# Performance work log

Hardware: AMD Instinct MI355X
Metric: run time of the kernel (lower is better)

## Reference

```python
import jax, jax.numpy as jnp
import numpy as np

B, N, H = 2, 2048, 256
NUM_HEADS = 8
HEAD_DIM = H // NUM_HEADS
E = 65536
NEG = -1e30
LN_EPS = 1e-5


def setup_inputs() -> dict:
    key = jax.random.key(0)
    ks = jax.random.split(key, 8)
    x = jax.random.normal(ks[0], (B, N, H), dtype=jnp.float32)
    edge_index = jax.random.randint(ks[1], (2, E), 0, N, dtype=jnp.int32)
    edge_weights = jax.random.uniform(ks[2], (E,), dtype=jnp.float32)
    s = 1.0 / np.sqrt(H)
    Wq = jax.random.normal(ks[3], (H, H), dtype=jnp.float32) * s
    Wk = jax.random.normal(ks[4], (H, H), dtype=jnp.float32) * s
    Wv = jax.random.normal(ks[5], (H, H), dtype=jnp.float32) * s
    Wo = jax.random.normal(ks[6], (H, H), dtype=jnp.float32) * s
    ln_gamma = jnp.ones((H,), dtype=jnp.float32)
    ln_beta = jnp.zeros((H,), dtype=jnp.float32)
    return {"node_embeddings": x, "edge_index": edge_index, "edge_weights": edge_weights,
            "Wq": Wq, "Wk": Wk, "Wv": Wv, "Wo": Wo, "ln_gamma": ln_gamma, "ln_beta": ln_beta}


def reference(node_embeddings, edge_index, edge_weights, Wq, Wk, Wv, Wo, ln_gamma, ln_beta):
    x = node_embeddings
    residual = x
    # torch Linear: y = x @ W.T
    def proj(W):
        y = jnp.einsum('bnd,ed->bne', x, W)
        return y.reshape(B, N, NUM_HEADS, HEAD_DIM).transpose(0, 2, 1, 3)  # [B,h,N,hd]
    Q, K, V = proj(Wq), proj(Wk), proj(Wv)
    scale = 1.0 / jnp.sqrt(jnp.float32(HEAD_DIM))
    scores = jnp.einsum('bhnd,bhmd->bhnm', Q, K) * scale  # [B,h,N,N]
    # adjacency mask from edge list
    mask = jnp.zeros((N, N), dtype=bool).at[edge_index[0], edge_index[1]].set(True)
    scores = jnp.where(mask[None, None], scores, NEG)
    w = jax.nn.softmax(scores, axis=-1)
    # rows with no edges: softmax over uniform NEG -> uniform; multiply by mask zeroes them
    # (equivalent to torch's -inf softmax + nan->0, but grad-safe)
    w = w * mask[None, None].astype(w.dtype)
    attn = jnp.einsum('bhnm,bhmd->bhnd', w, V)
    attn = attn.transpose(0, 2, 1, 3).reshape(B, N, H)
    out = jnp.einsum('bnd,ed->bne', attn, Wo)
    y = out + residual
    mu = jnp.mean(y, axis=-1, keepdims=True)
    var = jnp.mean(jnp.square(y - mu), axis=-1, keepdims=True)
    y = (y - mu) / jnp.sqrt(var + LN_EPS) * ln_gamma + ln_beta
    return y
```

## Files before the change

kernel.cpp:

```cpp
#include <hip/hip_runtime.h>
#include <math.h>

#define Bb 2
#define Nn 2048
#define Hh 256
#define NH 8
#define HD 32
#define NEDGE 65536
#define LN_EPS 1e-5f
#define MW 64

typedef __bf16 bf16_t;
typedef bf16_t bf16x8 __attribute__((ext_vector_type(8)));
typedef bf16_t bf16x4 __attribute__((ext_vector_type(4)));
typedef float f32x4 __attribute__((ext_vector_type(4)));

__global__ void build_mask_kernel(const int* __restrict__ ei, unsigned int* __restrict__ mask) {
    int e = blockIdx.x * blockDim.x + threadIdx.x;
    if (e >= NEDGE) return;
    int src = ei[e];
    int dst = ei[NEDGE + e];
    atomicOr(&mask[src * MW + (dst >> 5)], 1u << (dst & 31));
}

__global__ __launch_bounds__(256) void cvt_zero_kernel(
    const float* __restrict__ s0, const float* __restrict__ s1, const float* __restrict__ s2,
    const float* __restrict__ s3, const float* __restrict__ s4,
    bf16_t* __restrict__ d0, bf16_t* __restrict__ d1, bf16_t* __restrict__ d2,
    bf16_t* __restrict__ d3, bf16_t* __restrict__ d4,
    uint4* __restrict__ mask4)
{
    int which = blockIdx.y;
    int i = blockIdx.x * blockDim.x + threadIdx.x;
    if (which == 5) {
        if (i < Nn * MW / 4) mask4[i] = make_uint4(0, 0, 0, 0);
        return;
    }
    const float* s = (which == 0) ? s0 : (which == 1) ? s1 : (which == 2) ? s2 : (which == 3) ? s3 : s4;
    bf16_t* d = (which == 0) ? d0 : (which == 1) ? d1 : (which == 2) ? d2 : (which == 3) ? d3 : d4;
    int n4 = (which == 0) ? (Bb * Nn * Hh / 4) : (Hh * Hh / 4);
    if (i >= n4) return;
    float4 v = ((const float4*)s)[i];
    bf16x4 o = {(bf16_t)v.x, (bf16_t)v.y, (bf16_t)v.z, (bf16_t)v.w};
    ((bf16x4*)d)[i] = o;
}

#define LDA2 72

__global__ __launch_bounds__(256) void qkv_gemm3_kernel(
    const bf16_t* __restrict__ xb,
    const bf16_t* __restrict__ Wqb, const bf16_t* __restrict__ Wkb, const bf16_t* __restrict__ Wvb,
    float* __restrict__ Qb, bf16_t* __restrict__ Kb16, bf16_t* __restrict__ Vb16)
{
    __shared__ bf16_t As[64 * LDA2];
    __shared__ bf16_t Ws[64 * LDA2];
    int t = threadIdx.x;
    int lane = t & 63, w = t >> 6;
    int wm = w & 1, wn = w >> 1;
    int ml = lane & 15, quad = lane >> 4;
    int m0 = blockIdx.x * 64;
    int wsel = blockIdx.y >> 2;
    const bf16_t* W = (wsel == 0) ? Wqb : ((wsel == 1) ? Wkb : Wvb);
    int n0 = (blockIdx.y & 3) * 64;
    int srow = t >> 3;
    int scol = (t & 7) * 8;
    f32x4 acc[2][2];
    f32x4 zero = {0.f, 0.f, 0.f, 0.f};
    acc[0][0] = zero; acc[0][1] = zero; acc[1][0] = zero; acc[1][1] = zero;

    for (int k0 = 0; k0 < Hh; k0 += 64) {
        bf16x8 a[2], b[2];
        #pragma unroll
        for (int s = 0; s < 2; ++s) {
            a[s] = *(const bf16x8*)(xb + (size_t)(m0 + srow + s * 32) * Hh + k0 + scol);
            b[s] = *(const bf16x8*)(W  + (size_t)(n0 + srow + s * 32) * Hh + k0 + scol);
        }
        __syncthreads();
        #pragma unroll
        for (int s = 0; s < 2; ++s) {
            *(bf16x8*)&As[(srow + s * 32) * LDA2 + scol] = a[s];
            *(bf16x8*)&Ws[(srow + s * 32) * LDA2 + scol] = b[s];
        }
        __syncthreads();
        #pragma unroll
        for (int kk = 0; kk < 64; kk += 32) {
            bf16x8 af[2], bfr[2];
            #pragma unroll
            for (int i = 0; i < 2; ++i) {
                af[i]  = *(const bf16x8*)&As[(wm * 32 + i * 16 + ml) * LDA2 + kk + quad * 8];
                bfr[i] = *(const bf16x8*)&Ws[(wn * 32 + i * 16 + ml) * LDA2 + kk + quad * 8];
            }
            #pragma unroll
            for (int i = 0; i < 2; ++i)
                #pragma unroll
                for (int j = 0; j < 2; ++j)
                    acc[i][j] = __builtin_amdgcn_mfma_f32_16x16x32_bf16(af[i], bfr[j], acc[i][j], 0, 0, 0);
        }
    }
    bf16_t* Ob16 = (wsel == 1) ? Kb16 : Vb16;
    #pragma unroll
    for (int i = 0; i < 2; ++i)
        #pragma unroll
        for (int j = 0; j < 2; ++j)
            #pragma unroll
            for (int r = 0; r < 4; ++r) {
                int mg = m0 + wm * 32 + i * 16 + quad * 4 + r;
                int ng = n0 + wn * 32 + j * 16 + ml;
                float v = acc[i][j][r];
                if (wsel == 0) Qb[(size_t)mg * Hh + ng] = v;
                else           Ob16[(size_t)mg * Hh + ng] = (bf16_t)v;
            }
}

__global__ __launch_bounds__(256) void attn5_kernel(
    const float* __restrict__ Qb, const bf16_t* __restrict__ Kb16, const bf16_t* __restrict__ Vb16,
    const unsigned int* __restrict__ mask, float* __restrict__ attnb)
{
    __shared__ unsigned short nbr[Nn];
    __shared__ float qs[Hh];
    __shared__ float sraw[32 * 9];
    __shared__ float scw[Hh];
    __shared__ float alpha_l[NH];
    __shared__ float linv_l[NH];
    __shared__ float obuf[4][Hh];
    __shared__ int nn_sh;
    int gid = blockIdx.x;
    int i = gid & (Nn - 1);
    int b = gid >> 11;
    int t = threadIdx.x;
    int h = t >> 5, dl = t & 31;
    int w = t >> 6, lane = t & 63;
    int hw = lane >> 3;

    if (t < 64) {
        unsigned int bits = mask[i * MW + t];
        int cnt = __popc(bits);
        int incl = cnt;
        #pragma unroll
        for (int off = 1; off < 64; off <<= 1) {
            int v = __shfl_up(incl, off, 64);
            if (t >= off) incl += v;
        }
        int idx = incl - cnt;
        unsigned int bb = bits;
        while (bb) {
            int bit = __ffs(bb) - 1;
            nbr[idx++] = (unsigned short)(t * 32 + bit);
            bb &= bb - 1;
        }
        if (t == 63) nn_sh = incl;
    }
    qs[t] = Qb[((size_t)((b << 11) + i)) * Hh + t];
    __syncthreads();
    int nn = nn_sh;

    float m_run = -1e30f, l_run = 0.f;
    float o0 = 0.f, o1 = 0.f, o2 = 0.f, o3 = 0.f;
    const float scale = 0.17677669529663687f;
    int nch = (nn + 31) >> 5;
    for (int c = 0; c < nch; ++c) {
        int base = c << 5;
        int lim = min(32, nn - base);
        float4 qv = *(const float4*)&qs[lane << 2];
        #pragma unroll
        for (int s = 0; s < 8; ++s) {
            int r = (s << 2) + w;
            if (r < lim) {
                int j = nbr[base + r];
                bf16x4 kv = *(const bf16x4*)(Kb16 + (((size_t)((b << 11) + j)) << 8) + (lane << 2));
                float p = fmaf((float)kv.x, qv.x, fmaf((float)kv.y, qv.y,
                          fmaf((float)kv.z, qv.z, (float)kv.w * qv.w)));
                p += __shfl_xor(p, 1, 64);
                p += __shfl_xor(p, 2, 64);
                p += __shfl_xor(p, 4, 64);
                if ((lane & 7) == 0) sraw[r * 9 + (lane >> 3)] = p * scale;
            }
        }
        __syncthreads();
        float s_val = (dl < lim) ? sraw[dl * 9 + h] : -1e30f;
        float mc = s_val;
        #pragma unroll
        for (int m = 1; m < 32; m <<= 1) mc = fmaxf(mc, __shfl_xor(mc, m, 64));
        float m_new = fmaxf(m_run, mc);
        float wgt = __expf(s_val - m_new);
        float sum = wgt;
        #pragma unroll
        for (int m = 1; m < 32; m <<= 1) sum += __shfl_xor(sum, m, 64);
        float alpha = __expf(m_run - m_new);
        l_run = l_run * alpha + sum;
        m_run = m_new;
        scw[t] = wgt;
        if (dl == 0) alpha_l[h] = alpha;
        __syncthreads();
        float av = alpha_l[hw];
        o0 *= av; o1 *= av; o2 *= av; o3 *= av;
        #pragma unroll
        for (int s = 0; s < 8; ++s) {
            int r = (s << 2) + w;
            if (r < lim) {
                int j = nbr[base + r];
                float wg = scw[(hw << 5) + r];
                bf16x4 vv = *(const bf16x4*)(Vb16 + (((size_t)((b << 11) + j)) << 8) + (lane << 2));
                o0 = fmaf(wg, (float)vv.x, o0);
                o1 = fmaf(wg, (float)vv.y, o1);
                o2 = fmaf(wg, (float)vv.z, o2);
                o3 = fmaf(wg, (float)vv.w, o3);
            }
        }
    }
    if (dl == 0) linv_l[h] = (l_run > 0.f) ? 1.f / l_run : 0.f;
    obuf[w][(lane << 2) + 0] = o0;
    obuf[w][(lane << 2) + 1] = o1;
    obuf[w][(lane << 2) + 2] = o2;
    obuf[w][(lane << 2) + 3] = o3;
    __syncthreads();
    float val = obuf[0][t] + obuf[1][t] + obuf[2][t] + obuf[3][t];
    attnb[(((size_t)((b << 11) + i)) << 8) + t] = val * linv_l[t >> 5];
}

__global__ __launch_bounds__(256) void out_ln_kernel(
    const float* __restrict__ attnb, const bf16_t* __restrict__ Wob,
    const float* __restrict__ x, const float* __restrict__ gamma,
    const float* __restrict__ beta, float* __restrict__ out)
{
    __shared__ bf16_t As[16 * LDA2];
    __shared__ __align__(16) char wbuf[256 * LDA2 * sizeof(bf16_t)];
    bf16_t* Ws = (bf16_t*)wbuf;
    float* yb = (float*)wbuf;
    int t = threadIdx.x;
    int lane = t & 63, w = t >> 6;
    int ml = lane & 15, quad = lane >> 4;
    int m0 = blockIdx.x * 16;
    f32x4 acc[4];
    f32x4 zero = {0.f, 0.f, 0.f, 0.f};
    acc[0] = zero; acc[1] = zero; acc[2] = zero; acc[3] = zero;
    int arow = t >> 4, acol = (t & 15) * 4;
    int wrow = t >> 3, wcol = (t & 7) * 8;

    for (int k0 = 0; k0 < Hh; k0 += 64) {
        float4 av = *(const float4*)(attnb + (size_t)(m0 + arow) * Hh + k0 + acol);
        bf16x8 wv[8];
        #pragma unroll
        for (int s = 0; s < 8; ++s)
            wv[s] = *(const bf16x8*)(Wob + (size_t)(wrow + s * 32) * Hh + k0 + wcol);
        __syncthreads();
        bf16x4 ac = {(bf16_t)av.x, (bf16_t)av.y, (bf16_t)av.z, (bf16_t)av.w};
        *(bf16x4*)&As[arow * LDA2 + acol] = ac;
        #pragma unroll
        for (int s = 0; s < 8; ++s)
            *(bf16x8*)&Ws[(wrow + s * 32) * LDA2 + wcol] = wv[s];
        __syncthreads();
        #pragma unroll
        for (int kk = 0; kk < 64; kk += 32) {
            bf16x8 af = *(const bf16x8*)&As[ml * LDA2 + kk + quad * 8];
            #pragma unroll
            for (int ct = 0; ct < 4; ++ct) {
                bf16x8 bfr = *(const bf16x8*)&Ws[(w * 64 + ct * 16 + ml) * LDA2 + kk + quad * 8];
                acc[ct] = __builtin_amdgcn_mfma_f32_16x16x32_bf16(af, bfr, acc[ct], 0, 0, 0);
            }
        }
    }
    __syncthreads();
    #pragma unroll
    for (int ct = 0; ct < 4; ++ct)
        #pragma unroll
        for (int r = 0; r < 4; ++r) {
            int row = quad * 4 + r;
            int col = w * 64 + ct * 16 + ml;
            yb[row * 260 + col] = acc[ct][r] + x[(size_t)(m0 + row) * Hh + col];
        }
    __syncthreads();
    for (int rr = 0; rr < 4; ++rr) {
        int row = w * 4 + rr;
        float4 v = *(const float4*)&yb[row * 260 + lane * 4];
        float sum = v.x + v.y + v.z + v.w;
        #pragma unroll
        for (int m = 1; m < 64; m <<= 1) sum += __shfl_xor(sum, m, 64);
        float mu = sum * (1.f / Hh);
        float4 d = {v.x - mu, v.y - mu, v.z - mu, v.w - mu};
        float ss = d.x * d.x + d.y * d.y + d.z * d.z + d.w * d.w;
        #pragma unroll
        for (int m = 1; m < 64; m <<= 1) ss += __shfl_xor(ss, m, 64);
        float r = rsqrtf(ss * (1.f / Hh) + LN_EPS);
        float4 g  = *(const float4*)(gamma + lane * 4);
        float4 bt = *(const float4*)(beta + lane * 4);
        float4 ov = {d.x * r * g.x + bt.x, d.y * r * g.y + bt.y,
                     d.z * r * g.z + bt.z, d.w * r * g.w + bt.w};
        *(float4*)(out + (size_t)(m0 + row) * Hh + lane * 4) = ov;
    }
}

extern "C" void kernel_launch(void* const* d_in, const int* in_sizes, int n_in,
                              void* d_out, int out_size, void* d_ws, size_t ws_size,
                              hipStream_t stream) {
    const float* x     = (const float*)d_in[0];
    const int*   ei    = (const int*)d_in[1];
    const float* Wq    = (const float*)d_in[3];
    const float* Wk    = (const float*)d_in[4];
    const float* Wv    = (const float*)d_in[5];
    const float* Wo    = (const float*)d_in[6];
    const float* gamma = (const float*)d_in[7];
    const float* beta  = (const float*)d_in[8];
    float* out = (float*)d_out;

    const int NTOK = Bb * Nn * Hh;
    float*  Qb    = (float*)d_ws;
    bf16_t* Kb16  = (bf16_t*)(Qb + NTOK);
    bf16_t* Vb16  = Kb16 + NTOK;
    float*  attnb = (float*)(Vb16 + NTOK);
    unsigned int* mask = (unsigned int*)(attnb + NTOK);
    bf16_t* xb  = (bf16_t*)(mask + Nn * MW);
    bf16_t* Wqb = xb + NTOK;
    bf16_t* Wkb = Wqb + Hh * Hh;
    bf16_t* Wvb = Wkb + Hh * Hh;
    bf16_t* Wob = Wvb + Hh * Hh;

    hipLaunchKernelGGL(cvt_zero_kernel, dim3(NTOK / 4 / 256, 6), dim3(256), 0, stream,
                       x, Wq, Wk, Wv, Wo, xb, Wqb, Wkb, Wvb, Wob, (uint4*)mask);
    hipLaunchKernelGGL(build_mask_kernel, dim3(NEDGE / 256), dim3(256), 0, stream, ei, mask);
    hipLaunchKernelGGL(qkv_gemm3_kernel, dim3((Bb * Nn) / 64, 12), dim3(256), 0, stream,
                       xb, Wqb, Wkb, Wvb, Qb, Kb16, Vb16);
    hipLaunchKernelGGL(attn5_kernel, dim3(Bb * Nn), dim3(256), 0, stream,
                       Qb, Kb16, Vb16, mask, attnb);
    hipLaunchKernelGGL(out_ln_kernel, dim3((Bb * Nn) / 16), dim3(256), 0, stream,
                       attnb, Wob, x, gamma, beta, out);
}
```

Measured before the change: 116.5 us.

## Fuse mask build into QKV GEMM and attention with output projection and LayerNorm

The separate mask-building kernel is folded into the QKV GEMM, with each thread doing one edge atomicOr before its GEMM work. The attention kernel now handles 4 query rows per block, keeps the attention outputs in LDS, and then runs the Wo projection plus residual and LayerNorm in the same block. This removes the attnb global round trip and two launches. Attention chunks grow from 32 to 64 neighbours. In exchange there are only 1024 attention blocks instead of 4096, rows are processed serially inside a block, and Wo is reloaded per block for an M=4 MFMA tile that wastes 3/4 of each 16-row tile.

```diff
diff --git a/kernel.cpp b/kernel.cpp
--- a/kernel.cpp
+++ b/kernel.cpp
@@ -5,23 +5,15 @@
 #define Nn 2048
 #define Hh 256
 #define NH 8
-#define HD 32
 #define NEDGE 65536
 #define LN_EPS 1e-5f
 #define MW 64
+#define LDA2 72
 
 typedef __bf16 bf16_t;
 typedef bf16_t bf16x8 __attribute__((ext_vector_type(8)));
 typedef bf16_t bf16x4 __attribute__((ext_vector_type(4)));
 typedef float f32x4 __attribute__((ext_vector_type(4)));
-
-__global__ void build_mask_kernel(const int* __restrict__ ei, unsigned int* __restrict__ mask) {
-    int e = blockIdx.x * blockDim.x + threadIdx.x;
-    if (e >= NEDGE) return;
-    int src = ei[e];
-    int dst = ei[NEDGE + e];
-    atomicOr(&mask[src * MW + (dst >> 5)], 1u << (dst & 31));
-}
 
 __global__ __launch_bounds__(256) void cvt_zero_kernel(
     const float* __restrict__ s0, const float* __restrict__ s1, const float* __restrict__ s2,
@@ -45,16 +37,21 @@
     ((bf16x4*)d)[i] = o;
 }
 
-#define LDA2 72
-
-__global__ __launch_bounds__(256) void qkv_gemm3_kernel(
+__global__ __launch_bounds__(256) void qkv_gemm_mask_kernel(
     const bf16_t* __restrict__ xb,
     const bf16_t* __restrict__ Wqb, const bf16_t* __restrict__ Wkb, const bf16_t* __restrict__ Wvb,
-    float* __restrict__ Qb, bf16_t* __restrict__ Kb16, bf16_t* __restrict__ Vb16)
+    float* __restrict__ Qb, bf16_t* __restrict__ Kb16, bf16_t* __restrict__ Vb16,
+    const int* __restrict__ ei, unsigned int* __restrict__ mask)
 {
     __shared__ bf16_t As[64 * LDA2];
     __shared__ bf16_t Ws[64 * LDA2];
     int t = threadIdx.x;
+    int linb = blockIdx.y * 64 + blockIdx.x;
+    int gtid = linb * 256 + t;
+    if (gtid < NEDGE) {
+        int src = ei[gtid], dst = ei[NEDGE + gtid];
+        atomicOr(&mask[src * MW + (dst >> 5)], 1u << (dst & 31));
+    }
     int lane = t & 63, w = t >> 6;
     int wm = w & 1, wn = w >> 1;
     int ml = lane & 15, quad = lane >> 4;
@@ -65,214 +62,222 @@
     int srow = t >> 3;
     int scol = (t & 7) * 8;
     f32x4 acc[2][2];
-    f32x4 zero = {0.f, 0.f, 0.f, 0.f};
-    acc[0][0] = zero; acc[0][1] = zero; acc[1][0] = zero; acc[1][1] = zero;
+    f32x4 zf = {0.f, 0.f, 0.f, 0.f};
+    acc[0][0] = zf; acc[0][1] = zf; acc[1][0] = zf; acc[1][1] = zf;
 
     for (int k0 = 0; k0 < Hh; k0 += 64) {
-        bf16x8 a[2], b[2];
-        #pragma unroll
-        for (int s = 0; s < 2; ++s) {
-            a[s] = *(const bf16x8*)(xb + (size_t)(m0 + srow + s * 32) * Hh + k0 + scol);
-            b[s] = *(const bf16x8*)(W  + (size_t)(n0 + srow + s * 32) * Hh + k0 + scol);
-        }
-        __syncthreads();
-        #pragma unroll
-        for (int s = 0; s < 2; ++s) {
-            *(bf16x8*)&As[(srow + s * 32) * LDA2 + scol] = a[s];
-            *(bf16x8*)&Ws[(srow + s * 32) * LDA2 + scol] = b[s];
-        }
+        bf16x8 a0 = *(const bf16x8*)(xb + (size_t)(m0 + srow) * Hh + k0 + scol);
+        bf16x8 a1 = *(const bf16x8*)(xb + (size_t)(m0 + srow + 32) * Hh + k0 + scol);
+        bf16x8 b0 = *(const bf16x8*)(W + (size_t)(n0 + srow) * Hh + k0 + scol);
+        bf16x8 b1 = *(const bf16x8*)(W + (size_t)(n0 + srow + 32) * Hh + k0 + scol);
+        __syncthreads();
+        *(bf16x8*)&As[srow * LDA2 + scol] = a0;
+        *(bf16x8*)&As[(srow + 32) * LDA2 + scol] = a1;
+        *(bf16x8*)&Ws[srow * LDA2 + scol] = b0;
+        *(bf16x8*)&Ws[(srow + 32) * LDA2 + scol] = b1;
         __syncthreads();
         #pragma unroll
         for (int kk = 0; kk < 64; kk += 32) {
             bf16x8 af[2], bfr[2];
             #pragma unroll
-            for (int i = 0; i < 2; ++i) {
-                af[i]  = *(const bf16x8*)&As[(wm * 32 + i * 16 + ml) * LDA2 + kk + quad * 8];
-                bfr[i] = *(const bf16x8*)&Ws[(wn * 32 + i * 16 + ml) * LDA2 + kk + quad * 8];
-            }
-            #pragma unroll
-            for (int i = 0; i < 2; ++i)
+            for (int i2 = 0; i2 < 2; ++i2) {
+                af[i2]  = *(const bf16x8*)&As[(wm * 32 + i2 * 16 + ml) * LDA2 + kk + quad * 8];
+                bfr[i2] = *(const bf16x8*)&Ws[(wn * 32 + i2 * 16 + ml) * LDA2 + kk + quad * 8];
+            }
+            #pragma unroll
+            for (int i2 = 0; i2 < 2; ++i2)
                 #pragma unroll
-                for (int j = 0; j < 2; ++j)
-                    acc[i][j] = __builtin_amdgcn_mfma_f32_16x16x32_bf16(af[i], bfr[j], acc[i][j], 0, 0, 0);
-        }
-    }
-    bf16_t* Ob16 = (wsel == 1) ? Kb16 : Vb16;
+                for (int j2 = 0; j2 < 2; ++j2)
+                    acc[i2][j2] = __builtin_amdgcn_mfma_f32_16x16x32_bf16(af[i2], bfr[j2], acc[i2][j2], 0, 0, 0);
+        }
+    }
     #pragma unroll
-    for (int i = 0; i < 2; ++i)
-        #pragma unroll
-        for (int j = 0; j < 2; ++j)
+    for (int i2 = 0; i2 < 2; ++i2)
+        #pragma unroll
+        for (int j2 = 0; j2 < 2; ++j2)
             #pragma unroll
             for (int r = 0; r < 4; ++r) {
-                int mg = m0 + wm * 32 + i * 16 + quad * 4 + r;
-                int ng = n0 + wn * 32 + j * 16 + ml;
-                float v = acc[i][j][r];
-                if (wsel == 0) Qb[(size_t)mg * Hh + ng] = v;
-                else           Ob16[(size_t)mg * Hh + ng] = (bf16_t)v;
+                int mg = m0 + wm * 32 + i2 * 16 + quad * 4 + r;
+                int ng = n0 + wn * 32 + j2 * 16 + ml;
+                float v = acc[i2][j2][r];
+                if (wsel == 0)      Qb[(size_t)mg * Hh + ng] = v;
+                else if (wsel == 1) Kb16[(size_t)mg * Hh + ng] = (bf16_t)v;
+                else                Vb16[(size_t)mg * Hh + ng] = (bf16_t)v;
             }
 }
 
-__global__ __launch_bounds__(256) void attn5_kernel(
+struct AttnLds {
+    float aout[4][Hh];
+    unsigned short nbr[Nn];
+    float qs[Hh];
+    float sraw[64 * 9];
+    float scw2[NH * 64];
+    float alpha_l[NH];
+    float linv_l[NH];
+    float obuf[4][Hh];
+    int nn_sh;
+};
+struct OlnLds {
+    float aout[4][Hh];
+    union { bf16_t Ws[64 * 136]; float yb[4][260]; } u2;
+};
+union FusedLds { AttnLds a; OlnLds o; };
+
+__global__ __launch_bounds__(256) void attn_out_ln_kernel(
     const float* __restrict__ Qb, const bf16_t* __restrict__ Kb16, const bf16_t* __restrict__ Vb16,
-    const unsigned int* __restrict__ mask, float* __restrict__ attnb)
-{
-    __shared__ unsigned short nbr[Nn];
-    __shared__ float qs[Hh];
-    __shared__ float sraw[32 * 9];
-    __shared__ float scw[Hh];
-    __shared__ float alpha_l[NH];
-    __shared__ float linv_l[NH];
-    __shared__ float obuf[4][Hh];
-    __shared__ int nn_sh;
-    int gid = blockIdx.x;
-    int i = gid & (Nn - 1);
-    int b = gid >> 11;
-    int t = threadIdx.x;
-    int h = t >> 5, dl = t & 31;
-    int w = t >> 6, lane = t & 63;
-    int hw = lane >> 3;
-
-    if (t < 64) {
-        unsigned int bits = mask[i * MW + t];
-        int cnt = __popc(bits);
-        int incl = cnt;
-        #pragma unroll
-        for (int off = 1; off < 64; off <<= 1) {
-            int v = __shfl_up(incl, off, 64);
-            if (t >= off) incl += v;
-        }
-        int idx = incl - cnt;
-        unsigned int bb = bits;
-        while (bb) {
-            int bit = __ffs(bb) - 1;
-            nbr[idx++] = (unsigned short)(t * 32 + bit);
-            bb &= bb - 1;
-        }
-        if (t == 63) nn_sh = incl;
-    }
-    qs[t] = Qb[((size_t)((b << 11) + i)) * Hh + t];
-    __syncthreads();
-    int nn = nn_sh;
-
-    float m_run = -1e30f, l_run = 0.f;
-    float o0 = 0.f, o1 = 0.f, o2 = 0.f, o3 = 0.f;
-    const float scale = 0.17677669529663687f;
-    int nch = (nn + 31) >> 5;
-    for (int c = 0; c < nch; ++c) {
-        int base = c << 5;
-        int lim = min(32, nn - base);
-        float4 qv = *(const float4*)&qs[lane << 2];
-        #pragma unroll
-        for (int s = 0; s < 8; ++s) {
-            int r = (s << 2) + w;
-            if (r < lim) {
-                int j = nbr[base + r];
-                bf16x4 kv = *(const bf16x4*)(Kb16 + (((size_t)((b << 11) + j)) << 8) + (lane << 2));
-                float p = fmaf((float)kv.x, qv.x, fmaf((float)kv.y, qv.y,
-                          fmaf((float)kv.z, qv.z, (float)kv.w * qv.w)));
-                p += __shfl_xor(p, 1, 64);
-                p += __shfl_xor(p, 2, 64);
-                p += __shfl_xor(p, 4, 64);
-                if ((lane & 7) == 0) sraw[r * 9 + (lane >> 3)] = p * scale;
-            }
-        }
-        __syncthreads();
-        float s_val = (dl < lim) ? sraw[dl * 9 + h] : -1e30f;
-        float mc = s_val;
-        #pragma unroll
-        for (int m = 1; m < 32; m <<= 1) mc = fmaxf(mc, __shfl_xor(mc, m, 64));
-        float m_new = fmaxf(m_run, mc);
-        float wgt = __expf(s_val - m_new);
-        float sum = wgt;
-        #pragma unroll
-        for (int m = 1; m < 32; m <<= 1) sum += __shfl_xor(sum, m, 64);
-        float alpha = __expf(m_run - m_new);
-        l_run = l_run * alpha + sum;
-        m_run = m_new;
-        scw[t] = wgt;
-        if (dl == 0) alpha_l[h] = alpha;
-        __syncthreads();
-        float av = alpha_l[hw];
-        o0 *= av; o1 *= av; o2 *= av; o3 *= av;
-        #pragma unroll
-        for (int s = 0; s < 8; ++s) {
-            int r = (s << 2) + w;
-            if (r < lim) {
-                int j = nbr[base + r];
-                float wg = scw[(hw << 5) + r];
-                bf16x4 vv = *(const bf16x4*)(Vb16 + (((size_t)((b << 11) + j)) << 8) + (lane << 2));
-                o0 = fmaf(wg, (float)vv.x, o0);
-                o1 = fmaf(wg, (float)vv.y, o1);
-                o2 = fmaf(wg, (float)vv.z, o2);
-                o3 = fmaf(wg, (float)vv.w, o3);
-            }
-        }
-    }
-    if (dl == 0) linv_l[h] = (l_run > 0.f) ? 1.f / l_run : 0.f;
-    obuf[w][(lane << 2) + 0] = o0;
-    obuf[w][(lane << 2) + 1] = o1;
-    obuf[w][(lane << 2) + 2] = o2;
-    obuf[w][(lane << 2) + 3] = o3;
-    __syncthreads();
-    float val = obuf[0][t] + obuf[1][t] + obuf[2][t] + obuf[3][t];
-    attnb[(((size_t)((b << 11) + i)) << 8) + t] = val * linv_l[t >> 5];
-}
-
-__global__ __launch_bounds__(256) void out_ln_kernel(
-    const float* __restrict__ attnb, const bf16_t* __restrict__ Wob,
+    const unsigned int* __restrict__ mask, const bf16_t* __restrict__ Wob,
     const float* __restrict__ x, const float* __restrict__ gamma,
     const float* __restrict__ beta, float* __restrict__ out)
 {
-    __shared__ bf16_t As[16 * LDA2];
-    __shared__ __align__(16) char wbuf[256 * LDA2 * sizeof(bf16_t)];
-    bf16_t* Ws = (bf16_t*)wbuf;
-    float* yb = (float*)wbuf;
-    int t = threadIdx.x;
+    __shared__ FusedLds u;
+    int blk = blockIdx.x, t = threadIdx.x;
     int lane = t & 63, w = t >> 6;
     int ml = lane & 15, quad = lane >> 4;
-    int m0 = blockIdx.x * 16;
-    f32x4 acc[4];
-    f32x4 zero = {0.f, 0.f, 0.f, 0.f};
-    acc[0] = zero; acc[1] = zero; acc[2] = zero; acc[3] = zero;
-    int arow = t >> 4, acol = (t & 15) * 4;
-    int wrow = t >> 3, wcol = (t & 7) * 8;
-
-    for (int k0 = 0; k0 < Hh; k0 += 64) {
-        float4 av = *(const float4*)(attnb + (size_t)(m0 + arow) * Hh + k0 + acol);
-        bf16x8 wv[8];
-        #pragma unroll
-        for (int s = 0; s < 8; ++s)
-            wv[s] = *(const bf16x8*)(Wob + (size_t)(wrow + s * 32) * Hh + k0 + wcol);
-        __syncthreads();
-        bf16x4 ac = {(bf16_t)av.x, (bf16_t)av.y, (bf16_t)av.z, (bf16_t)av.w};
-        *(bf16x4*)&As[arow * LDA2 + acol] = ac;
-        #pragma unroll
-        for (int s = 0; s < 8; ++s)
-            *(bf16x8*)&Ws[(wrow + s * 32) * LDA2 + wcol] = wv[s];
-        __syncthreads();
-        #pragma unroll
-        for (int kk = 0; kk < 64; kk += 32) {
-            bf16x8 af = *(const bf16x8*)&As[ml * LDA2 + kk + quad * 8];
-            #pragma unroll
-            for (int ct = 0; ct < 4; ++ct) {
-                bf16x8 bfr = *(const bf16x8*)&Ws[(w * 64 + ct * 16 + ml) * LDA2 + kk + quad * 8];
-                acc[ct] = __builtin_amdgcn_mfma_f32_16x16x32_bf16(af, bfr, acc[ct], 0, 0, 0);
-            }
-        }
+    int h = t >> 5, dl = t & 31;
+    int hw = lane >> 3;
+    const float scale = 0.17677669529663687f;
+
+    for (int rr = 0; rr < 4; ++rr) {
+        int ri = blk * 4 + rr;
+        int b = ri >> 11, i = ri & (Nn - 1);
+        __syncthreads();
+        if (t < 64) {
+            unsigned int bits = mask[i * MW + t];
+            int cnt = __popc(bits);
+            int incl = cnt;
+            #pragma unroll
+            for (int off = 1; off < 64; off <<= 1) {
+                int v = __shfl_up(incl, off, 64);
+                if (t >= off) incl += v;
+            }
+            int idx = incl - cnt;
+            unsigned int bb = bits;
+            while (bb) {
+                int bit = __ffs(bb) - 1;
+                u.a.nbr[idx++] = (unsigned short)(t * 32 + bit);
+                bb &= bb - 1;
+            }
+            if (t == 63) u.a.nn_sh = incl;
+        }
+        u.a.qs[t] = Qb[(size_t)ri * Hh + t];
+        __syncthreads();
+        int nn = u.a.nn_sh;
+
+        float m_run = -1e30f, l_run = 0.f;
+        float o0 = 0.f, o1 = 0.f, o2 = 0.f, o3 = 0.f;
+        int nch = (nn + 63) >> 6;
+        for (int c = 0; c < nch; ++c) {
+            int base = c << 6;
+            int lim = min(64, nn - base);
+            float4 qv = *(const float4*)&u.a.qs[lane << 2];
+            #pragma unroll
+            for (int s = 0; s < 16; ++s) {
+                int r = (s << 2) + w;
+                if (r < lim) {
+                    int j = u.a.nbr[base + r];
+                    bf16x4 kv = *(const bf16x4*)(Kb16 + (((size_t)((b << 11) + j)) << 8) + (lane << 2));
+                    float p = fmaf((float)kv.x, qv.x, fmaf((float)kv.y, qv.y,
+                              fmaf((float)kv.z, qv.z, (float)kv.w * qv.w)));
+                    p += __shfl_xor(p, 1, 64);
+                    p += __shfl_xor(p, 2, 64);
+                    p += __shfl_xor(p, 4, 64);
+                    if ((lane & 7) == 0) u.a.sraw[r * 9 + (lane >> 3)] = p * scale;
+                }
+            }
+            __syncthreads();
+            float s0 = (dl < lim) ? u.a.sraw[dl * 9 + h] : -1e30f;
+            float s1 = (dl + 32 < lim) ? u.a.sraw[(dl + 32) * 9 + h] : -1e30f;
+            float mc = fmaxf(s0, s1);
+            #pragma unroll
+            for (int m = 1; m < 32; m <<= 1) mc = fmaxf(mc, __shfl_xor(mc, m, 64));
+            float m_new = fmaxf(m_run, mc);
+            float w0 = __expf(s0 - m_new), w1 = __expf(s1 - m_new);
+            float sum = w0 + w1;
+            #pragma unroll
+            for (int m = 1; m < 32; m <<= 1) sum += __shfl_xor(sum, m, 64);
+            float alpha = __expf(m_run - m_new);
+            l_run = l_run * alpha + sum;
+            m_run = m_new;
+            u.a.scw2[h * 64 + dl] = w0;
+            u.a.scw2[h * 64 + dl + 32] = w1;
+            if (dl == 0) u.a.alpha_l[h] = alpha;
+            __syncthreads();
+            float av = u.a.alpha_l[hw];
+            o0 *= av; o1 *= av; o2 *= av; o3 *= av;
+            #pragma unroll
+            for (int s = 0; s < 16; ++s) {
+                int r = (s << 2) + w;
+                if (r < lim) {
+                    int j = u.a.nbr[base + r];
+                    float wg = u.a.scw2[hw * 64 + r];
+                    bf16x4 vv = *(const bf16x4*)(Vb16 + (((size_t)((b << 11) + j)) << 8) + (lane << 2));
+                    o0 = fmaf(wg, (float)vv.x, o0);
+                    o1 = fmaf(wg, (float)vv.y, o1);
+                    o2 = fmaf(wg, (float)vv.z, o2);
+                    o3 = fmaf(wg, (float)vv.w, o3);
+                }
+            }
+            __syncthreads();
+        }
+        if (dl == 0) u.a.linv_l[h] = (l_run > 0.f) ? 1.f / l_run : 0.f;
+        u.a.obuf[w][(lane << 2) + 0] = o0;
+        u.a.obuf[w][(lane << 2) + 1] = o1;
+        u.a.obuf[w][(lane << 2) + 2] = o2;
+        u.a.obuf[w][(lane << 2) + 3] = o3;
+        __syncthreads();
+        float val = u.a.obuf[0][t] + u.a.obuf[1][t] + u.a.obuf[2][t] + u.a.obuf[3][t];
+        u.a.aout[rr][t] = val * u.a.linv_l[t >> 5];
     }
     __syncthreads();
-    #pragma unroll
-    for (int ct = 0; ct < 4; ++ct)
-        #pragma unroll
-        for (int r = 0; r < 4; ++r) {
-            int row = quad * 4 + r;
-            int col = w * 64 + ct * 16 + ml;
-            yb[row * 260 + col] = acc[ct][r] + x[(size_t)(m0 + row) * Hh + col];
-        }
-    __syncthreads();
-    for (int rr = 0; rr < 4; ++rr) {
-        int row = w * 4 + rr;
-        float4 v = *(const float4*)&yb[row * 260 + lane * 4];
+
+    {
+        int mlr = ml & 3;
+        bf16x8 af[8];
+        #pragma unroll
+        for (int kc = 0; kc < 8; ++kc) {
+            float4 a0 = *(const float4*)&u.o.aout[mlr][kc * 32 + quad * 8];
+            float4 a1 = *(const float4*)&u.o.aout[mlr][kc * 32 + quad * 8 + 4];
+            bf16x8 f = {(bf16_t)a0.x, (bf16_t)a0.y, (bf16_t)a0.z, (bf16_t)a0.w,
+                        (bf16_t)a1.x, (bf16_t)a1.y, (bf16_t)a1.z, (bf16_t)a1.w};
+            af[kc] = f;
+        }
+        int wr = t >> 2, wc = (t & 3) * 32;
+        f32x4 acc[4];
+        f32x4 zf = {0.f, 0.f, 0.f, 0.f};
+        acc[0] = zf; acc[1] = zf; acc[2] = zf; acc[3] = zf;
+        #pragma unroll
+        for (int nc = 0; nc < 4; ++nc) {
+            #pragma unroll
+            for (int kcp = 0; kcp < 2; ++kcp) {
+                bf16x8 wv0 = *(const bf16x8*)(Wob + (size_t)(nc * 64 + wr) * Hh + kcp * 128 + wc);
+                bf16x8 wv1 = *(const bf16x8*)(Wob + (size_t)(nc * 64 + wr) * Hh + kcp * 128 + wc + 8);
+                bf16x8 wv2 = *(const bf16x8*)(Wob + (size_t)(nc * 64 + wr) * Hh + kcp * 128 + wc + 16);
+                bf16x8 wv3 = *(const bf16x8*)(Wob + (size_t)(nc * 64 + wr) * Hh + kcp * 128 + wc + 24);
+                __syncthreads();
+                *(bf16x8*)&u.o.u2.Ws[wr * 136 + wc +  0] = wv0;
+                *(bf16x8*)&u.o.u2.Ws[wr * 136 + wc +  8] = wv1;
+                *(bf16x8*)&u.o.u2.Ws[wr * 136 + wc + 16] = wv2;
+                *(bf16x8*)&u.o.u2.Ws[wr * 136 + wc + 24] = wv3;
+                __syncthreads();
+                #pragma unroll
+                for (int k2 = 0; k2 < 4; ++k2) {
+                    bf16x8 bfr = *(const bf16x8*)&u.o.u2.Ws[(w * 16 + ml) * 136 + k2 * 32 + quad * 8];
+                    acc[nc] = __builtin_amdgcn_mfma_f32_16x16x32_bf16(af[kcp * 4 + k2], bfr, acc[nc], 0, 0, 0);
+                }
+            }
+        }
+        __syncthreads();
+        if (quad == 0) {
+            #pragma unroll
+            for (int nc = 0; nc < 4; ++nc)
+                #pragma unroll
+                for (int r = 0; r < 4; ++r) {
+                    int col = nc * 64 + w * 16 + ml;
+                    u.o.u2.yb[r][col] = acc[nc][r] + x[(size_t)(blk * 4 + r) * Hh + col];
+                }
+        }
+        __syncthreads();
+        float4 v = *(const float4*)&u.o.u2.yb[w][lane * 4];
         float sum = v.x + v.y + v.z + v.w;
         #pragma unroll
         for (int m = 1; m < 64; m <<= 1) sum += __shfl_xor(sum, m, 64);
@@ -286,7 +291,7 @@
         float4 bt = *(const float4*)(beta + lane * 4);
         float4 ov = {d.x * r * g.x + bt.x, d.y * r * g.y + bt.y,
                      d.z * r * g.z + bt.z, d.w * r * g.w + bt.w};
-        *(float4*)(out + (size_t)(m0 + row) * Hh + lane * 4) = ov;
+        *(float4*)(out + (size_t)(blk * 4 + w) * Hh + lane * 4) = ov;
     }
 }
 
@@ -304,11 +309,10 @@
     float* out = (float*)d_out;
 
     const int NTOK = Bb * Nn * Hh;
-    float*  Qb    = (float*)d_ws;
-    bf16_t* Kb16  = (bf16_t*)(Qb + NTOK);
-    bf16_t* Vb16  = Kb16 + NTOK;
-    float*  attnb = (float*)(Vb16 + NTOK);
-    unsigned int* mask = (unsigned int*)(attnb + NTOK);
+    float*  Qb   = (float*)d_ws;
+    bf16_t* Kb16 = (bf16_t*)(Qb + NTOK);
+    bf16_t* Vb16 = Kb16 + NTOK;
+    unsigned int* mask = (unsigned int*)(Vb16 + NTOK);
     bf16_t* xb  = (bf16_t*)(mask + Nn * MW);
     bf16_t* Wqb = xb + NTOK;
     bf16_t* Wkb = Wqb + Hh * Hh;
@@ -317,11 +321,8 @@
 
     hipLaunchKernelGGL(cvt_zero_kernel, dim3(NTOK / 4 / 256, 6), dim3(256), 0, stream,
                        x, Wq, Wk, Wv, Wo, xb, Wqb, Wkb, Wvb, Wob, (uint4*)mask);
-    hipLaunchKernelGGL(build_mask_kernel, dim3(NEDGE / 256), dim3(256), 0, stream, ei, mask);
-    hipLaunchKernelGGL(qkv_gemm3_kernel, dim3((Bb * Nn) / 64, 12), dim3(256), 0, stream,
-                       xb, Wqb, Wkb, Wvb, Qb, Kb16, Vb16);
-    hipLaunchKernelGGL(attn5_kernel, dim3(Bb * Nn), dim3(256), 0, stream,
-                       Qb, Kb16, Vb16, mask, attnb);
-    hipLaunchKernelGGL(out_ln_kernel, dim3((Bb * Nn) / 16), dim3(256), 0, stream,
-                       attnb, Wob, x, gamma, beta, out);
+    hipLaunchKernelGGL(qkv_gemm_mask_kernel, dim3(64, 12), dim3(256), 0, stream,
+                       xb, Wqb, Wkb, Wvb, Qb, Kb16, Vb16, ei, mask);
+    hipLaunchKernelGGL(attn_out_ln_kernel, dim3(Bb * Nn / 4), dim3(256), 0, stream,
+                       Qb, Kb16, Vb16, mask, Wob, x, gamma, beta, out);
 }
```

After: 138.4 us. +18.8%, slower.

## Fuse fp32-to-bf16 conversion and mask build into QKV GEMM, drop launches

Applied to the files above, without the earlier changes.

Removes the separate conversion and mask-build kernels. The QKV GEMM now loads fp32 x and weights directly, converts them to bf16 while staging into shared memory, and builds the adjacency bitmask with atomics in the same launch. A memset replaces the mask zeroing. The attention kernel drops its per-row branches by clamping neighbor indices, reuses one shared buffer, and prefetches Q. The output GEMM reads fp32 Wo directly. The aim is fewer launches and fewer bf16 intermediate round-trips, at the cost of redundant fp32 loads and conversions in each GEMM block. Because the mask is built inside the GEMM launch, the attention kernel depends on launch ordering to see a finished mask.

```diff
diff --git a/kernel.cpp b/kernel.cpp
--- a/kernel.cpp
+++ b/kernel.cpp
@@ -5,133 +5,113 @@
 #define Nn 2048
 #define Hh 256
 #define NH 8
-#define HD 32
 #define NEDGE 65536
 #define LN_EPS 1e-5f
 #define MW 64
+#define LDA2 72
 
 typedef __bf16 bf16_t;
 typedef bf16_t bf16x8 __attribute__((ext_vector_type(8)));
 typedef bf16_t bf16x4 __attribute__((ext_vector_type(4)));
 typedef float f32x4 __attribute__((ext_vector_type(4)));
 
-__global__ void build_mask_kernel(const int* __restrict__ ei, unsigned int* __restrict__ mask) {
-    int e = blockIdx.x * blockDim.x + threadIdx.x;
-    if (e >= NEDGE) return;
-    int src = ei[e];
-    int dst = ei[NEDGE + e];
-    atomicOr(&mask[src * MW + (dst >> 5)], 1u << (dst & 31));
-}
-
-__global__ __launch_bounds__(256) void cvt_zero_kernel(
-    const float* __restrict__ s0, const float* __restrict__ s1, const float* __restrict__ s2,
-    const float* __restrict__ s3, const float* __restrict__ s4,
-    bf16_t* __restrict__ d0, bf16_t* __restrict__ d1, bf16_t* __restrict__ d2,
-    bf16_t* __restrict__ d3, bf16_t* __restrict__ d4,
-    uint4* __restrict__ mask4)
-{
-    int which = blockIdx.y;
-    int i = blockIdx.x * blockDim.x + threadIdx.x;
-    if (which == 5) {
-        if (i < Nn * MW / 4) mask4[i] = make_uint4(0, 0, 0, 0);
-        return;
-    }
-    const float* s = (which == 0) ? s0 : (which == 1) ? s1 : (which == 2) ? s2 : (which == 3) ? s3 : s4;
-    bf16_t* d = (which == 0) ? d0 : (which == 1) ? d1 : (which == 2) ? d2 : (which == 3) ? d3 : d4;
-    int n4 = (which == 0) ? (Bb * Nn * Hh / 4) : (Hh * Hh / 4);
-    if (i >= n4) return;
-    float4 v = ((const float4*)s)[i];
+__device__ __forceinline__ bf16x4 cvt4(float4 v) {
     bf16x4 o = {(bf16_t)v.x, (bf16_t)v.y, (bf16_t)v.z, (bf16_t)v.w};
-    ((bf16x4*)d)[i] = o;
-}
-
-#define LDA2 72
-
-__global__ __launch_bounds__(256) void qkv_gemm3_kernel(
-    const bf16_t* __restrict__ xb,
-    const bf16_t* __restrict__ Wqb, const bf16_t* __restrict__ Wkb, const bf16_t* __restrict__ Wvb,
-    float* __restrict__ Qb, bf16_t* __restrict__ Kb16, bf16_t* __restrict__ Vb16)
+    return o;
+}
+
+__global__ __launch_bounds__(256) void qkv_gemm_mask_kernel(
+    const float* __restrict__ x,
+    const float* __restrict__ Wq, const float* __restrict__ Wk, const float* __restrict__ Wv,
+    float* __restrict__ Qb, bf16_t* __restrict__ Kb16, bf16_t* __restrict__ Vb16,
+    const int* __restrict__ ei, unsigned int* __restrict__ mask)
 {
     __shared__ bf16_t As[64 * LDA2];
     __shared__ bf16_t Ws[64 * LDA2];
     int t = threadIdx.x;
+    int linb = blockIdx.y * 64 + blockIdx.x;
+    int gtid = linb * 256 + t;
+    if (gtid < NEDGE) {
+        int src = ei[gtid], dst = ei[NEDGE + gtid];
+        atomicOr(&mask[src * MW + (dst >> 5)], 1u << (dst & 31));
+    }
     int lane = t & 63, w = t >> 6;
     int wm = w & 1, wn = w >> 1;
     int ml = lane & 15, quad = lane >> 4;
     int m0 = blockIdx.x * 64;
     int wsel = blockIdx.y >> 2;
-    const bf16_t* W = (wsel == 0) ? Wqb : ((wsel == 1) ? Wkb : Wvb);
+    const float* W = (wsel == 0) ? Wq : ((wsel == 1) ? Wk : Wv);
     int n0 = (blockIdx.y & 3) * 64;
-    int srow = t >> 3;
-    int scol = (t & 7) * 8;
+    int srow = t >> 4;
+    int scol = (t & 15) * 4;
     f32x4 acc[2][2];
-    f32x4 zero = {0.f, 0.f, 0.f, 0.f};
-    acc[0][0] = zero; acc[0][1] = zero; acc[1][0] = zero; acc[1][1] = zero;
+    f32x4 zf = {0.f, 0.f, 0.f, 0.f};
+    acc[0][0] = zf; acc[0][1] = zf; acc[1][0] = zf; acc[1][1] = zf;
 
     for (int k0 = 0; k0 < Hh; k0 += 64) {
-        bf16x8 a[2], b[2];
-        #pragma unroll
-        for (int s = 0; s < 2; ++s) {
-            a[s] = *(const bf16x8*)(xb + (size_t)(m0 + srow + s * 32) * Hh + k0 + scol);
-            b[s] = *(const bf16x8*)(W  + (size_t)(n0 + srow + s * 32) * Hh + k0 + scol);
-        }
-        __syncthreads();
-        #pragma unroll
-        for (int s = 0; s < 2; ++s) {
-            *(bf16x8*)&As[(srow + s * 32) * LDA2 + scol] = a[s];
-            *(bf16x8*)&Ws[(srow + s * 32) * LDA2 + scol] = b[s];
+        float4 av[4], wv4[4];
+        #pragma unroll
+        for (int u = 0; u < 4; ++u) {
+            av[u]  = *(const float4*)(x + (size_t)(m0 + u * 16 + srow) * Hh + k0 + scol);
+            wv4[u] = *(const float4*)(W + (size_t)(n0 + u * 16 + srow) * Hh + k0 + scol);
+        }
+        __syncthreads();
+        #pragma unroll
+        for (int u = 0; u < 4; ++u) {
+            *(bf16x4*)&As[(u * 16 + srow) * LDA2 + scol] = cvt4(av[u]);
+            *(bf16x4*)&Ws[(u * 16 + srow) * LDA2 + scol] = cvt4(wv4[u]);
         }
         __syncthreads();
         #pragma unroll
         for (int kk = 0; kk < 64; kk += 32) {
             bf16x8 af[2], bfr[2];
             #pragma unroll
-            for (int i = 0; i < 2; ++i) {
-                af[i]  = *(const bf16x8*)&As[(wm * 32 + i * 16 + ml) * LDA2 + kk + quad * 8];
-                bfr[i] = *(const bf16x8*)&Ws[(wn * 32 + i * 16 + ml) * LDA2 + kk + quad * 8];
+            for (int i2 = 0; i2 < 2; ++i2) {
+                af[i2]  = *(const bf16x8*)&As[(wm * 32 + i2 * 16 + ml) * LDA2 + kk + quad * 8];
+                bfr[i2] = *(const bf16x8*)&Ws[(wn * 32 + i2 * 16 + ml) * LDA2 + kk + quad * 8];
             }
             #pragma unroll
-            for (int i = 0; i < 2; ++i)
+            for (int i2 = 0; i2 < 2; ++i2)
                 #pragma unroll
-                for (int j = 0; j < 2; ++j)
-                    acc[i][j] = __builtin_amdgcn_mfma_f32_16x16x32_bf16(af[i], bfr[j], acc[i][j], 0, 0, 0);
-        }
-    }
-    bf16_t* Ob16 = (wsel == 1) ? Kb16 : Vb16;
+                for (int j2 = 0; j2 < 2; ++j2)
+                    acc[i2][j2] = __builtin_amdgcn_mfma_f32_16x16x32_bf16(af[i2], bfr[j2], acc[i2][j2], 0, 0, 0);
+        }
+    }
     #pragma unroll
-    for (int i = 0; i < 2; ++i)
-        #pragma unroll
-        for (int j = 0; j < 2; ++j)
+    for (int i2 = 0; i2 < 2; ++i2)
+        #pragma unroll
+        for (int j2 = 0; j2 < 2; ++j2)
             #pragma unroll
             for (int r = 0; r < 4; ++r) {
-                int mg = m0 + wm * 32 + i * 16 + quad * 4 + r;
-                int ng = n0 + wn * 32 + j * 16 + ml;
-                float v = acc[i][j][r];
-                if (wsel == 0) Qb[(size_t)mg * Hh + ng] = v;
-                else           Ob16[(size_t)mg * Hh + ng] = (bf16_t)v;
+                int mg = m0 + wm * 32 + i2 * 16 + quad * 4 + r;
+                int ng = n0 + wn * 32 + j2 * 16 + ml;
+                float v = acc[i2][j2][r];
+                if (wsel == 0)      Qb[(size_t)mg * Hh + ng] = v;
+                else if (wsel == 1) Kb16[(size_t)mg * Hh + ng] = (bf16_t)v;
+                else                Vb16[(size_t)mg * Hh + ng] = (bf16_t)v;
             }
 }
 
-__global__ __launch_bounds__(256) void attn5_kernel(
+__global__ __launch_bounds__(256) void attn6_kernel(
     const float* __restrict__ Qb, const bf16_t* __restrict__ Kb16, const bf16_t* __restrict__ Vb16,
     const unsigned int* __restrict__ mask, float* __restrict__ attnb)
 {
     __shared__ unsigned short nbr[Nn];
     __shared__ float qs[Hh];
-    __shared__ float sraw[32 * 9];
-    __shared__ float scw[Hh];
+    __shared__ float sw[32 * 9];
     __shared__ float alpha_l[NH];
     __shared__ float linv_l[NH];
     __shared__ float obuf[4][Hh];
     __shared__ int nn_sh;
     int gid = blockIdx.x;
     int i = gid & (Nn - 1);
-    int b = gid >> 11;
     int t = threadIdx.x;
     int h = t >> 5, dl = t & 31;
     int w = t >> 6, lane = t & 63;
     int hw = lane >> 3;
-
+    int kvbase = (gid >> 11) << 11;
+
+    float qreg = Qb[(size_t)gid * Hh + t];
     if (t < 64) {
         unsigned int bits = mask[i * MW + t];
         int cnt = __popc(bits);
@@ -150,7 +130,7 @@
         }
         if (t == 63) nn_sh = incl;
     }
-    qs[t] = Qb[((size_t)((b << 11) + i)) * Hh + t];
+    qs[t] = qreg;
     __syncthreads();
     int nn = nn_sh;
 
@@ -165,19 +145,17 @@
         #pragma unroll
         for (int s = 0; s < 8; ++s) {
             int r = (s << 2) + w;
-            if (r < lim) {
-                int j = nbr[base + r];
-                bf16x4 kv = *(const bf16x4*)(Kb16 + (((size_t)((b << 11) + j)) << 8) + (lane << 2));
-                float p = fmaf((float)kv.x, qv.x, fmaf((float)kv.y, qv.y,
-                          fmaf((float)kv.z, qv.z, (float)kv.w * qv.w)));
-                p += __shfl_xor(p, 1, 64);
-                p += __shfl_xor(p, 2, 64);
-                p += __shfl_xor(p, 4, 64);
-                if ((lane & 7) == 0) sraw[r * 9 + (lane >> 3)] = p * scale;
-            }
-        }
-        __syncthreads();
-        float s_val = (dl < lim) ? sraw[dl * 9 + h] : -1e30f;
+            int j = nbr[min(base + r, nn - 1)];
+            bf16x4 kv = *(const bf16x4*)(Kb16 + (((size_t)(kvbase + j)) << 8) + (lane << 2));
+            float p = fmaf((float)kv.x, qv.x, fmaf((float)kv.y, qv.y,
+                      fmaf((float)kv.z, qv.z, (float)kv.w * qv.w)));
+            p += __shfl_xor(p, 1, 64);
+            p += __shfl_xor(p, 2, 64);
+            p += __shfl_xor(p, 4, 64);
+            if ((lane & 7) == 0 && r < lim) sw[r * 9 + (lane >> 3)] = p * scale;
+        }
+        __syncthreads();
+        float s_val = (dl < lim) ? sw[dl * 9 + h] : -1e30f;
         float mc = s_val;
         #pragma unroll
         for (int m = 1; m < 32; m <<= 1) mc = fmaxf(mc, __shfl_xor(mc, m, 64));
@@ -189,7 +167,7 @@
         float alpha = __expf(m_run - m_new);
         l_run = l_run * alpha + sum;
         m_run = m_new;
-        scw[t] = wgt;
+        sw[dl * 9 + h] = wgt;
         if (dl == 0) alpha_l[h] = alpha;
         __syncthreads();
         float av = alpha_l[hw];
@@ -197,29 +175,26 @@
         #pragma unroll
         for (int s = 0; s < 8; ++s) {
             int r = (s << 2) + w;
-            if (r < lim) {
-                int j = nbr[base + r];
-                float wg = scw[(hw << 5) + r];
-                bf16x4 vv = *(const bf16x4*)(Vb16 + (((size_t)((b << 11) + j)) << 8) + (lane << 2));
-                o0 = fmaf(wg, (float)vv.x, o0);
-                o1 = fmaf(wg, (float)vv.y, o1);
-                o2 = fmaf(wg, (float)vv.z, o2);
-                o3 = fmaf(wg, (float)vv.w, o3);
-            }
-        }
+            int j = nbr[min(base + r, nn - 1)];
+            float wg = sw[r * 9 + hw];
+            bf16x4 vv = *(const bf16x4*)(Vb16 + (((size_t)(kvbase + j)) << 8) + (lane << 2));
+            o0 = fmaf(wg, (float)vv.x, o0);
+            o1 = fmaf(wg, (float)vv.y, o1);
+            o2 = fmaf(wg, (float)vv.z, o2);
+            o3 = fmaf(wg, (float)vv.w, o3);
+        }
+        __syncthreads();
     }
     if (dl == 0) linv_l[h] = (l_run > 0.f) ? 1.f / l_run : 0.f;
-    obuf[w][(lane << 2) + 0] = o0;
-    obuf[w][(lane << 2) + 1] = o1;
-    obuf[w][(lane << 2) + 2] = o2;
-    obuf[w][(lane << 2) + 3] = o3;
+    float4 ov = {o0, o1, o2, o3};
+    *(float4*)&obuf[w][lane << 2] = ov;
     __syncthreads();
     float val = obuf[0][t] + obuf[1][t] + obuf[2][t] + obuf[3][t];
-    attnb[(((size_t)((b << 11) + i)) << 8) + t] = val * linv_l[t >> 5];
+    attnb[((size_t)gid << 8) + t] = val * linv_l[t >> 5];
 }
 
 __global__ __launch_bounds__(256) void out_ln_kernel(
-    const float* __restrict__ attnb, const bf16_t* __restrict__ Wob,
+    const float* __restrict__ attnb, const float* __restrict__ Wo,
     const float* __restrict__ x, const float* __restrict__ gamma,
     const float* __restrict__ beta, float* __restrict__ out)
 {
@@ -232,23 +207,26 @@
     int ml = lane & 15, quad = lane >> 4;
     int m0 = blockIdx.x * 16;
     f32x4 acc[4];
-    f32x4 zero = {0.f, 0.f, 0.f, 0.f};
-    acc[0] = zero; acc[1] = zero; acc[2] = zero; acc[3] = zero;
+    f32x4 zf = {0.f, 0.f, 0.f, 0.f};
+    acc[0] = zf; acc[1] = zf; acc[2] = zf; acc[3] = zf;
     int arow = t >> 4, acol = (t & 15) * 4;
     int wrow = t >> 3, wcol = (t & 7) * 8;
 
     for (int k0 = 0; k0 < Hh; k0 += 64) {
         float4 av = *(const float4*)(attnb + (size_t)(m0 + arow) * Hh + k0 + acol);
-        bf16x8 wv[8];
-        #pragma unroll
-        for (int s = 0; s < 8; ++s)
-            wv[s] = *(const bf16x8*)(Wob + (size_t)(wrow + s * 32) * Hh + k0 + wcol);
-        __syncthreads();
-        bf16x4 ac = {(bf16_t)av.x, (bf16_t)av.y, (bf16_t)av.z, (bf16_t)av.w};
-        *(bf16x4*)&As[arow * LDA2 + acol] = ac;
-        #pragma unroll
-        for (int s = 0; s < 8; ++s)
-            *(bf16x8*)&Ws[(wrow + s * 32) * LDA2 + wcol] = wv[s];
+        float4 wa[8], wb[8];
+        #pragma unroll
+        for (int s = 0; s < 8; ++s) {
+            wa[s] = *(const float4*)(Wo + (size_t)(wrow + s * 32) * Hh + k0 + wcol);
+            wb[s] = *(const float4*)(Wo + (size_t)(wrow + s * 32) * Hh + k0 + wcol + 4);
+        }
+        __syncthreads();
+        *(bf16x4*)&As[arow * LDA2 + acol] = cvt4(av);
+        #pragma unroll
+        for (int s = 0; s < 8; ++s) {
+            *(bf16x4*)&Ws[(wrow + s * 32) * LDA2 + wcol]     = cvt4(wa[s]);
+            *(bf16x4*)&Ws[(wrow + s * 32) * LDA2 + wcol + 4] = cvt4(wb[s]);
+        }
         __syncthreads();
         #pragma unroll
         for (int kk = 0; kk < 64; kk += 32) {
@@ -309,19 +287,12 @@
     bf16_t* Vb16  = Kb16 + NTOK;
     float*  attnb = (float*)(Vb16 + NTOK);
     unsigned int* mask = (unsigned int*)(attnb + NTOK);
-    bf16_t* xb  = (bf16_t*)(mask + Nn * MW);
-    bf16_t* Wqb = xb + NTOK;
-    bf16_t* Wkb = Wqb + Hh * Hh;
-    bf16_t* Wvb = Wkb + Hh * Hh;
-    bf16_t* Wob = Wvb + Hh * Hh;
-
-    hipLaunchKernelGGL(cvt_zero_kernel, dim3(NTOK / 4 / 256, 6), dim3(256), 0, stream,
-                       x, Wq, Wk, Wv, Wo, xb, Wqb, Wkb, Wvb, Wob, (uint4*)mask);
-    hipLaunchKernelGGL(build_mask_kernel, dim3(NEDGE / 256), dim3(256), 0, stream, ei, mask);
-    hipLaunchKernelGGL(qkv_gemm3_kernel, dim3((Bb * Nn) / 64, 12), dim3(256), 0, stream,
-                       xb, Wqb, Wkb, Wvb, Qb, Kb16, Vb16);
-    hipLaunchKernelGGL(attn5_kernel, dim3(Bb * Nn), dim3(256), 0, stream,
+
+    hipMemsetAsync(mask, 0, Nn * MW * sizeof(unsigned int), stream);
+    hipLaunchKernelGGL(qkv_gemm_mask_kernel, dim3(64, 12), dim3(256), 0, stream,
+                       x, Wq, Wk, Wv, Qb, Kb16, Vb16, ei, mask);
+    hipLaunchKernelGGL(attn6_kernel, dim3(Bb * Nn), dim3(256), 0, stream,
                        Qb, Kb16, Vb16, mask, attnb);
     hipLaunchKernelGGL(out_ln_kernel, dim3((Bb * Nn) / 16), dim3(256), 0, stream,
-                       attnb, Wob, x, gamma, beta, out);
-}
+                       attnb, Wo, x, gamma, beta, out);
+}
```

Measured after the change: 118.3 us. Within noise of the previous version (+1.6%).
